# Kernel optimization log

Measured on AMD Instinct MI355X. Metric: run time of the kernel, lower is better.

Reference implementation:

```python
import jax, jax.numpy as jnp
import numpy as np
from jax.ops import segment_sum, segment_max

N = 20000   # nodes
E = 320000  # edges (no self loops; conv adds them)
G = 64      # graphs in batch
D = 128     # embed dim
H = 64      # GATConv out channels (heads=1)
L = 6       # number of conv/mlp blocks


def setup_inputs() -> dict:
    key = jax.random.key(0)
    ks = jax.random.split(key, 24)
    x_idx = jax.random.randint(ks[0], (N,), 0, 128)
    src = jax.random.randint(ks[1], (E,), 0, N)
    dst = jax.random.randint(ks[2], (E,), 0, N)
    dst = jnp.where(src == dst, (dst + 1) % N, dst)  # remove_self_loops semantics
    edge_index = jnp.stack([src, dst])
    edge_attr_idx = jax.random.randint(ks[3], (E,), 0, 128)
    batch = (jnp.arange(N) * G) // N  # sorted graph ids, ~312 nodes/graph
    s = 0.1
    r = lambda k, shp: jax.random.normal(k, shp, dtype=jnp.float32) * s
    return {
        'x_idx': x_idx, 'edge_index': edge_index, 'edge_attr_idx': edge_attr_idx, 'batch': batch,
        'emb': r(ks[4], (128, D)),
        'conv_W': r(ks[5], (L, D, H)), 'conv_We': r(ks[6], (L, D, H)),
        'conv_att_src': r(ks[7], (L, H)), 'conv_att_dst': r(ks[8], (L, H)),
        'conv_att_edge': r(ks[9], (L, H)), 'conv_b': jnp.zeros((L, H), jnp.float32),
        'mlp_W1': r(ks[10], (L, H, H)), 'mlp_b1': jnp.zeros((L, H), jnp.float32),
        'mlp_W2': r(ks[11], (L, H, H)), 'mlp_b2': jnp.zeros((L, H), jnp.float32),
        'mlp_W3': r(ks[12], (L, H, D)), 'mlp_b3': jnp.zeros((L, D), jnp.float32),
        'g1_W1': r(ks[13], (D, H)), 'g1_b1': jnp.zeros((H,), jnp.float32),
        'g1_W2': r(ks[14], (H, 1)), 'g1_b2': jnp.zeros((1,), jnp.float32),
        'g2_W1': r(ks[15], (D, H)), 'g2_b1': jnp.zeros((H,), jnp.float32),
        'g2_W2': r(ks[16], (H, D)), 'g2_b2': jnp.zeros((D,), jnp.float32),
        'p_W1': r(ks[17], (D, H)), 'p_b1': jnp.zeros((H,), jnp.float32),
        'p_W2': r(ks[18], (H, H)), 'p_b2': jnp.zeros((H,), jnp.float32),
        'p_W3': r(ks[19], (H, 1)), 'p_b3': jnp.zeros((1,), jnp.float32),
    }


def _mlp3(x, W1, b1, W2, b2, W3, b3):
    h = jax.nn.relu(x @ W1 + b1)
    h = jax.nn.relu(h @ W2 + b2)
    return h @ W3 + b3


def reference(x_idx, edge_index, edge_attr_idx, batch, emb, conv_W, conv_We,
              conv_att_src, conv_att_dst, conv_att_edge, conv_b,
              mlp_W1, mlp_b1, mlp_W2, mlp_b2, mlp_W3, mlp_b3,
              g1_W1, g1_b1, g1_W2, g1_b2, g2_W1, g2_b1, g2_W2, g2_b2,
              p_W1, p_b1, p_W2, p_b2, p_W3, p_b3):
    n = x_idx.shape[0]
    x = emb[x_idx]                 # [N,128]
    e = emb[edge_attr_idx]         # [E,128]
    src, dst = edge_index[0], edge_index[1]
    # add_self_loops with fill_value='mean': loop attr = mean of incoming edge attrs
    deg = segment_sum(jnp.ones((e.shape[0],), x.dtype), dst, num_segments=n)
    loop_attr = segment_sum(e, dst, num_segments=n) / jnp.maximum(deg, 1.0)[:, None]
    e_full = jnp.concatenate([e, loop_attr], axis=0)             # [E+N,128]
    ar = jnp.arange(n)
    src_f = jnp.concatenate([src, ar])
    dst_f = jnp.concatenate([dst, ar])

    def gat_conv(x, i):
        h = x @ conv_W[i]                       # [N,64]
        ep = e_full @ conv_We[i]                # [E+N,64]
        a_s = h @ conv_att_src[i]               # [N]
        a_d = h @ conv_att_dst[i]               # [N]
        a_e = ep @ conv_att_edge[i]             # [E+N]
        logit = jax.nn.leaky_relu(a_s[src_f] + a_d[dst_f] + a_e, 0.2)
        m = segment_max(logit, dst_f, num_segments=n)
        w = jnp.exp(logit - m[dst_f])
        denom = segment_sum(w, dst_f, num_segments=n)
        alpha = w / denom[dst_f]
        out = segment_sum(h[src_f] * alpha[:, None], dst_f, num_segments=n)
        return out + conv_b[i]

    jkn = []
    for i in range(L):  # dropout is identity at inference
        x = gat_conv(x, i)
        x = _mlp3(x, mlp_W1[i], mlp_b1[i], mlp_W2[i], mlp_b2[i], mlp_W3[i], mlp_b3[i])
        jkn.append(x)
    jkn = jnp.stack(jkn)                                  # [6,N,128]
    ms = jnp.sqrt(jnp.sum(jnp.square(jkn), axis=2))       # [6,N]
    ni = jnp.argmax(ms, axis=0)                           # [N]
    feature = jnp.take_along_axis(jkn, ni[None, :, None], axis=0)[0]  # [N,128]

    # per-graph attention pooling (vectorized over the per-graph loop)
    h1 = (jax.nn.relu(feature @ g1_W1 + g1_b1) @ g1_W2 + g1_b2)[:, 0]  # [N]
    m = segment_max(h1, batch, num_segments=G)
    w = jnp.exp(h1 - m[batch])
    attn = w / segment_sum(w, batch, num_segments=G)[batch]            # softmax per graph
    h2 = jax.nn.relu(feature @ g2_W1 + g2_b1) @ g2_W2 + g2_b2          # [N,128]
    counts = segment_sum(jnp.ones((n,), feature.dtype), batch, num_segments=G)
    hg = segment_sum(attn[:, None] * h2, batch, num_segments=G) / counts[:, None]  # [G,128]

    out = _mlp3(hg, p_W1, p_b1, p_W2, p_b2, p_W3, p_b3)   # [G,1]
    return out[:, 0]
```

## Files before the change

### kernel.cpp

```cpp
#include <hip/hip_runtime.h>
#include <math.h>

__device__ __forceinline__ float lrelu(float x){ return x > 0.0f ? x : 0.2f*x; }
__device__ __forceinline__ float bcastf(float v, int l){
    return __int_as_float(__builtin_amdgcn_readlane(__float_as_int(v), l));
}


__global__ void k_count(const int* __restrict__ dst, int* __restrict__ cnt, int E){
    int e = blockIdx.x*256 + threadIdx.x;
    if(e < E) atomicAdd(&cnt[dst[e]], 1);
}

__global__ __launch_bounds__(1024) void k_scan(const int* __restrict__ cnt, int* __restrict__ rowptr, int n){
    __shared__ int ws[16];
    __shared__ int carrysh;
    int t = threadIdx.x, lane = t & 63, wv = t >> 6;
    if(t==0){ carrysh = 0; rowptr[0] = 0; }
    __syncthreads();
    for(int base=0; base<n; base+=1024){
        int i = base + t;
        int v = (i<n) ? cnt[i] : 0;
        int s = v;
        #pragma unroll
        for(int off=1; off<64; off<<=1){ int u = __shfl_up(s, off, 64); if(lane>=off) s += u; }
        if(lane==63) ws[wv] = s;
        __syncthreads();
        if(t < 16){
            int u = ws[t];
            #pragma unroll
            for(int off=1; off<16; off<<=1){ int u2 = __shfl_up(u, off, 16); if(t>=off) u += u2; }
            ws[t] = u;
        }
        __syncthreads();
        int carry = carrysh;
        int wbase = wv ? ws[wv-1] : 0;
        if(i<n) rowptr[i+1] = carry + wbase + s;
        int total = ws[15];
        __syncthreads();
        if(t==0) carrysh = carry + total;
        __syncthreads();
    }
}

__global__ void k_scatter(const int* __restrict__ dst, const int* __restrict__ rowptr,
                          int* __restrict__ cnt2, int* __restrict__ eid, int E){
    int e = blockIdx.x*256 + threadIdx.x;
    if(e >= E) return;
    int d = dst[e];
    int p = rowptr[d] + atomicAdd(&cnt2[d], 1);
    eid[p] = e;
}

__global__ __launch_bounds__(256) void k_sortb(const int* __restrict__ rowptr, int* __restrict__ eid, int n){
    int node = blockIdx.x*4 + (threadIdx.x>>6);
    if(node >= n) return;
    int lane = threadIdx.x & 63;
    int b = rowptr[node], e = rowptr[node+1];
    int nj = e - b;
    if(nj <= 1) return;
    if(nj <= 64){
        int v = (lane < nj) ? eid[b+lane] : 0x7fffffff;
        for(int k=2; k<=64; k<<=1){
            for(int j=k>>1; j>0; j>>=1){
                int vv = __shfl_xor(v, j, 64);
                bool up = ((lane & k) == 0);
                bool lower = ((lane & j) == 0);
                int mn = min(v,vv), mx = max(v,vv);
                v = (lower == up) ? mn : mx;
            }
        }
        if(lane < nj) eid[b+lane] = v;
    } else if(lane == 0){
        for(int i=b+1; i<e; i++){
            int key = eid[i]; int j = i-1;
            while(j>=b && eid[j] > key){ eid[j+1] = eid[j]; j--; }
            eid[j+1] = key;
        }
    }
}

__global__ __launch_bounds__(256) void k_ae(const int* __restrict__ eid, const int* __restrict__ src,
                     const int* __restrict__ eattr, const float* __restrict__ emb,
                     const float* __restrict__ We, const float* __restrict__ atte,
                     int* __restrict__ csrsrc, float* __restrict__ ae, int E){
    __shared__ float wv[6*128];
    for(int i=threadIdx.x; i<768; i+=256){
        int l = i>>7, k = i&127;
        const float* w = We + ((size_t)l*128 + k)*64;
        const float* a = atte + l*64;
        float s = 0.f;
        #pragma unroll 8
        for(int c=0;c<64;c++) s += w[c]*a[c];
        wv[i] = s;
    }
    __syncthreads();
    int p = blockIdx.x*256 + threadIdx.x;
    if(p >= E) return;
    int e = eid[p];
    csrsrc[p] = src[e];
    const float4* er = (const float4*)(emb + (size_t)eattr[e]*128);
    float acc[6] = {0,0,0,0,0,0};
    for(int k=0;k<32;k++){
        float4 v = er[k];
        #pragma unroll
        for(int l=0;l<6;l++){
            const float* w = wv + l*128 + k*4;
            acc[l] += v.x*w[0] + v.y*w[1] + v.z*w[2] + v.w*w[3];
        }
    }
    #pragma unroll
    for(int l=0;l<6;l++) ae[(size_t)l*E + p] = acc[l];
}


__global__ __launch_bounds__(512) void k_hx(const int* __restrict__ xidx, const float* __restrict__ emb,
        const float* __restrict__ W, const float* __restrict__ atts, const float* __restrict__ attd,
        float* __restrict__ h, float* __restrict__ as_, float* __restrict__ ad_, int n){
    __shared__ float xs[64][129];
    __shared__ float hs[64][65];
    __shared__ float redA[8][64], redB[8][64];
    int base = blockIdx.x*64;
    int t = threadIdx.x;
    {
        int r = t>>3, c0 = (t&7)*16;
        if(base + r < n){
            const float4* srcp = (const float4*)(emb + (size_t)xidx[base+r]*128 + c0);
            #pragma unroll
            for(int q=0;q<4;q++){
                float4 v = srcp[q];
                xs[r][c0+q*4+0]=v.x; xs[r][c0+q*4+1]=v.y; xs[r][c0+q*4+2]=v.z; xs[r][c0+q*4+3]=v.w;
            }
        } else {
            #pragma unroll
            for(int q=0;q<16;q++) xs[r][c0+q] = 0.f;
        }
    }
    __syncthreads();
    int lane = t & 63;
    int wid = __builtin_amdgcn_readfirstlane(t >> 6);
    int cb = wid*8;
    float acc[8] = {0,0,0,0,0,0,0,0};
    for(int k=0;k<128;k++){
        float xv = xs[lane][k];
        #pragma unroll
        for(int cc=0;cc<8;cc++) acc[cc] = fmaf(xv, W[k*64 + cb + cc], acc[cc]);
    }
    float pa=0.f, pd=0.f;
    #pragma unroll
    for(int cc=0;cc<8;cc++){
        hs[lane][cb+cc] = acc[cc];
        pa += acc[cc]*atts[cb+cc];
        pd += acc[cc]*attd[cb+cc];
    }
    redA[wid][lane]=pa; redB[wid][lane]=pd;
    __syncthreads();
    {
        int r = t>>3, c0 = (t&7)*8;
        if(base + r < n){
            float* dst = h + (size_t)(base+r)*64 + c0;
            #pragma unroll
            for(int q=0;q<8;q++) dst[q] = hs[r][c0+q];
        }
    }
    if(t < 64 && base + t < n){
        float sa=0.f, sd=0.f;
        #pragma unroll
        for(int w=0;w<8;w++){ sa += redA[w][t]; sd += redB[w][t]; }
        as_[base+t] = sa; ad_[base+t] = sd;
    }
}


__global__ __launch_bounds__(256) void k_gat(const float* __restrict__ h,
        const float* __restrict__ as_, const float* __restrict__ ad_,
        const float* __restrict__ ae, const int* __restrict__ rowptr,
        const int* __restrict__ csrsrc, const float* __restrict__ bias,
        float* __restrict__ o, int n){
    int node = blockIdx.x*4 + (threadIdx.x>>6);
    if(node >= n) return;
    int lane = threadIdx.x & 63;
    int b = rowptr[node], e = rowptr[node+1];
    float adv = ad_[node];
    float m = -1e30f, d = 0.f, sumae = 0.f;
    float a0=0.f, a1=0.f, a2=0.f, a3=0.f;
    for(int j0=b; j0<e; j0+=64){
        int nj = min(64, e-j0);
        int sj = 0; float aev = 0.f, lg = -1e30f;
        if(lane < nj){
            sj  = csrsrc[j0+lane];
            aev = ae[j0+lane];
            lg  = lrelu(as_[sj] + adv + aev);
        }
        float cm = lg, sa = aev;
        #pragma unroll
        for(int off=32; off; off>>=1){ cm = fmaxf(cm, __shfl_xor(cm,off,64)); sa += __shfl_xor(sa,off,64); }
        sumae += sa;
        float nm = fmaxf(m, cm);
        float w = (lane<nj) ? expf(lg-nm) : 0.f;
        float ws = w;
        #pragma unroll
        for(int off=32; off; off>>=1) ws += __shfl_xor(ws,off,64);
        float scale = (m > -1e29f) ? expf(m-nm) : 0.f;
        d = d*scale + ws;
        a0*=scale; a1*=scale; a2*=scale; a3*=scale;
        int j = 0;
        for(; j+3<nj; j+=4){
            a0 = fmaf(bcastf(w,j+0), h[(size_t)__builtin_amdgcn_readlane(sj,j+0)*64 + lane], a0);
            a1 = fmaf(bcastf(w,j+1), h[(size_t)__builtin_amdgcn_readlane(sj,j+1)*64 + lane], a1);
            a2 = fmaf(bcastf(w,j+2), h[(size_t)__builtin_amdgcn_readlane(sj,j+2)*64 + lane], a2);
            a3 = fmaf(bcastf(w,j+3), h[(size_t)__builtin_amdgcn_readlane(sj,j+3)*64 + lane], a3);
        }
        for(; j<nj; j++)
            a0 = fmaf(bcastf(w,j), h[(size_t)__builtin_amdgcn_readlane(sj,j)*64 + lane], a0);
        m = nm;
    }
    int deg = e - b;
    float ael = sumae / fmaxf((float)deg, 1.f);
    float ls = lrelu(as_[node] + adv + ael);
    float nm = fmaxf(m, ls);
    float scale = (m > -1e29f) ? expf(m-nm) : 0.f;
    float wl = expf(ls-nm);
    d = d*scale + wl;
    float acc = (a0+a1)+(a2+a3);
    acc = acc*scale + wl*h[(size_t)node*64 + lane];
    o[(size_t)node*64 + lane] = acc/d + bias[lane];
}


__global__ __launch_bounds__(512) void k_dense(
    const float* __restrict__ o,
    const float* __restrict__ W1, const float* __restrict__ b1,
    const float* __restrict__ W2, const float* __restrict__ b2,
    const float* __restrict__ W3, const float* __restrict__ b3,
    float* __restrict__ bestF, float* __restrict__ bestMs, int layer,
    const float* __restrict__ Wn, const float* __restrict__ atts, const float* __restrict__ attd,
    float* __restrict__ hn, float* __restrict__ asn, float* __restrict__ adn_,
    const float* __restrict__ A, const float* __restrict__ g1b1,
    const float* __restrict__ w2, const float* __restrict__ g1b2,
    const float* __restrict__ B, const float* __restrict__ g2b1,
    const float* __restrict__ C, const float* __restrict__ g2b2,
    float* __restrict__ h1, float* __restrict__ h2,
    int n, int last)
{
    __shared__ float o_s[64][65];
    __shared__ float t1[64][65];
    __shared__ float xs[64][129];
    __shared__ float redA[8][64], redB[8][64];
    __shared__ unsigned char updf[64];
    int base = blockIdx.x*64;
    int t = threadIdx.x, lane = t & 63;
    int wid = __builtin_amdgcn_readfirstlane(t >> 6);

    {
        int r = t>>3, c0 = (t&7)*8;
        if(base + r < n){
            const float4* srcp = (const float4*)(o + (size_t)(base+r)*64 + c0);
            float4 v0 = srcp[0], v1 = srcp[1];
            o_s[r][c0+0]=v0.x; o_s[r][c0+1]=v0.y; o_s[r][c0+2]=v0.z; o_s[r][c0+3]=v0.w;
            o_s[r][c0+4]=v1.x; o_s[r][c0+5]=v1.y; o_s[r][c0+6]=v1.z; o_s[r][c0+7]=v1.w;
        } else {
            #pragma unroll
            for(int q=0;q<8;q++) o_s[r][c0+q] = 0.f;
        }
    }
    __syncthreads();

    {
        int cb = wid*8;
        float acc[8];
        #pragma unroll
        for(int cc=0;cc<8;cc++) acc[cc] = b1[cb+cc];
        for(int k=0;k<64;k++){
            float ov = o_s[lane][k];
            #pragma unroll
            for(int cc=0;cc<8;cc++) acc[cc] = fmaf(ov, W1[k*64 + cb + cc], acc[cc]);
        }
        #pragma unroll
        for(int cc=0;cc<8;cc++) t1[lane][cb+cc] = fmaxf(acc[cc], 0.f);
    }
    __syncthreads();

    {
        int cb = wid*8;
        float acc[8];
        #pragma unroll
        for(int cc=0;cc<8;cc++) acc[cc] = b2[cb+cc];
        for(int k=0;k<64;k++){
            float tv = t1[lane][k];
            #pragma unroll
            for(int cc=0;cc<8;cc++) acc[cc] = fmaf(tv, W2[k*64 + cb + cc], acc[cc]);
        }
        __syncthreads();
        #pragma unroll
        for(int cc=0;cc<8;cc++) o_s[lane][cb+cc] = fmaxf(acc[cc], 0.f);
    }
    __syncthreads();

    {
        int cb = wid*16;
        float acc[16];
        #pragma unroll
        for(int cc=0;cc<16;cc++) acc[cc] = b3[cb+cc];
        for(int k=0;k<64;k++){
            float tv = o_s[lane][k];
            #pragma unroll
            for(int cc=0;cc<16;cc++) acc[cc] = fmaf(tv, W3[k*128 + cb + cc], acc[cc]);
        }
        float ms = 0.f;
        #pragma unroll
        for(int cc=0;cc<16;cc++){ xs[lane][cb+cc] = acc[cc]; ms += acc[cc]*acc[cc]; }
        redA[wid][lane] = ms;
    }
    __syncthreads();

    if(t < 64){
        int node = base + t; bool u = false;
        if(node < n){
            float ms = 0.f;
            #pragma unroll
            for(int w=0;w<8;w++) ms += redA[w][t];
            u = (layer==0) || (ms > bestMs[node]);
            if(u) bestMs[node] = ms;
        }
        updf[t] = u ? 1 : 0;
    }
    __syncthreads();

    if(!last){
        {
            int r = t>>3, c0 = (t&7)*16;
            if(updf[r] && base + r < n){
                float* dst = bestF + (size_t)(base+r)*128 + c0;
                #pragma unroll
                for(int q=0;q<16;q++) dst[q] = xs[r][c0+q];
            }
        }
        {
            int cb = wid*8;
            float acc[8] = {0,0,0,0,0,0,0,0};
            for(int k=0;k<128;k++){
                float xv = xs[lane][k];
                #pragma unroll
                for(int cc=0;cc<8;cc++) acc[cc] = fmaf(xv, Wn[k*64 + cb + cc], acc[cc]);
            }
            float pa=0.f, pd=0.f;
            #pragma unroll
            for(int cc=0;cc<8;cc++){
                t1[lane][cb+cc] = acc[cc];
                pa += acc[cc]*atts[cb+cc];
                pd += acc[cc]*attd[cb+cc];
            }
            redA[wid][lane]=pa; redB[wid][lane]=pd;
        }
        __syncthreads();
        {
            int r = t>>3, c0 = (t&7)*8;
            if(base + r < n){
                float* dst = hn + (size_t)(base+r)*64 + c0;
                #pragma unroll
                for(int q=0;q<8;q++) dst[q] = t1[r][c0+q];
            }
        }
        if(t < 64 && base + t < n){
            float sa=0.f, sd=0.f;
            #pragma unroll
            for(int w=0;w<8;w++){ sa += redA[w][t]; sd += redB[w][t]; }
            asn[base+t] = sa; adn_[base+t] = sd;
        }
        return;
    }

    {
        int r = t>>3, c0 = (t&7)*16;
        if(!updf[r] && base + r < n){
            const float4* srcp = (const float4*)(bestF + (size_t)(base+r)*128 + c0);
            #pragma unroll
            for(int q=0;q<4;q++){
                float4 v = srcp[q];
                xs[r][c0+q*4+0]=v.x; xs[r][c0+q*4+1]=v.y; xs[r][c0+q*4+2]=v.z; xs[r][c0+q*4+3]=v.w;
            }
        }
    }
    __syncthreads();
    if(wid < 4){
        int cb = wid*16;
        float acc[16];
        #pragma unroll
        for(int cc=0;cc<16;cc++) acc[cc] = g1b1[cb+cc];
        for(int k=0;k<128;k++){
            float fv = xs[lane][k];
            #pragma unroll
            for(int cc=0;cc<16;cc++) acc[cc] = fmaf(fv, A[k*64 + cb + cc], acc[cc]);
        }
        float pp = 0.f;
        #pragma unroll
        for(int cc=0;cc<16;cc++) pp += fmaxf(acc[cc],0.f)*w2[cb+cc];
        redA[wid][lane] = pp;
    } else {
        int cb = (wid-4)*16;
        float acc[16];
        #pragma unroll
        for(int cc=0;cc<16;cc++) acc[cc] = g2b1[cb+cc];
        for(int k=0;k<128;k++){
            float fv = xs[lane][k];
            #pragma unroll
            for(int cc=0;cc<16;cc++) acc[cc] = fmaf(fv, B[k*64 + cb + cc], acc[cc]);
        }
        #pragma unroll
        for(int cc=0;cc<16;cc++) t1[lane][cb+cc] = fmaxf(acc[cc],0.f);
    }
    __syncthreads();
    if(t < 64 && base + t < n)
        h1[base+t] = redA[0][t]+redA[1][t]+redA[2][t]+redA[3][t] + g1b2[0];
    {
        int cb = wid*16;
        float acc[16];
        #pragma unroll
        for(int cc=0;cc<16;cc++) acc[cc] = g2b2[cb+cc];
        for(int k=0;k<64;k++){
            float tv = t1[lane][k];
            #pragma unroll
            for(int cc=0;cc<16;cc++) acc[cc] = fmaf(tv, C[k*128 + cb + cc], acc[cc]);
        }
        __syncthreads();
        #pragma unroll
        for(int cc=0;cc<16;cc++) xs[lane][cb+cc] = acc[cc];
    }
    __syncthreads();
    {
        int r = t>>3, c0 = (t&7)*16;
        if(base + r < n){
            float* dst = h2 + (size_t)(base+r)*128 + c0;
            #pragma unroll
            for(int q=0;q<16;q++) dst[q] = xs[r][c0+q];
        }
    }
}


__global__ __launch_bounds__(128) void k_pool2(const float* __restrict__ h1, const float* __restrict__ h2,
                      float* __restrict__ wbuf,
                      const float* __restrict__ pW1, const float* __restrict__ pb1,
                      const float* __restrict__ pW2, const float* __restrict__ pb2,
                      const float* __restrict__ pW3, const float* __restrict__ pb3,
                      float* __restrict__ out, int n, int G){
    __shared__ float sh[128];
    __shared__ float hgrow[128];
    int g = blockIdx.x, tid = threadIdx.x;
    int start = (g*n + G-1)/G, end = ((g+1)*n + G-1)/G;
    float lm = -1e30f;
    for(int i=start+tid; i<end; i+=128) lm = fmaxf(lm, h1[i]);
    sh[tid]=lm; __syncthreads();
    for(int off=64; off; off>>=1){ if(tid<off) sh[tid]=fmaxf(sh[tid],sh[tid+off]); __syncthreads(); }
    float m = sh[0]; __syncthreads();
    float lsum = 0.f;
    for(int i=start+tid; i<end; i+=128){ float w = expf(h1[i]-m); wbuf[i]=w; lsum+=w; }
    sh[tid]=lsum; __syncthreads();
    for(int off=64; off; off>>=1){ if(tid<off) sh[tid]+=sh[tid+off]; __syncthreads(); }
    float denom = sh[0];
    float a0=0.f,a1=0.f,a2=0.f,a3=0.f;
    int i = start;
    for(; i+3<end; i+=4){
        a0 = fmaf(wbuf[i+0], h2[(size_t)(i+0)*128 + tid], a0);
        a1 = fmaf(wbuf[i+1], h2[(size_t)(i+1)*128 + tid], a1);
        a2 = fmaf(wbuf[i+2], h2[(size_t)(i+2)*128 + tid], a2);
        a3 = fmaf(wbuf[i+3], h2[(size_t)(i+3)*128 + tid], a3);
    }
    for(; i<end; i++) a0 = fmaf(wbuf[i], h2[(size_t)i*128 + tid], a0);
    float acc = (a0+a1)+(a2+a3);
    hgrow[tid] = acc/denom/(float)(end-start);
    __syncthreads();
    if(tid < 64){
        float t1v = pb1[tid];
        for(int k=0;k<128;k++) t1v = fmaf(hgrow[k], pW1[k*64+tid], t1v);
        t1v = fmaxf(t1v, 0.f);
        float t2v = pb2[tid];
        for(int k=0;k<64;k++) t2v = fmaf(__shfl(t1v,k,64), pW2[k*64+tid], t2v);
        t2v = fmaxf(t2v, 0.f);
        float s = t2v * pW3[tid];
        #pragma unroll
        for(int off=32; off; off>>=1) s += __shfl_xor(s,off,64);
        if(tid==0) out[g] = s + pb3[0];
    }
}

extern "C" void kernel_launch(void* const* d_in, const int* in_sizes, int n_in,
                              void* d_out, int out_size, void* d_ws, size_t ws_size,
                              hipStream_t stream){
    const int*   x_idx   = (const int*)  d_in[0];
    const int*   eindex  = (const int*)  d_in[1];
    const int*   eattr   = (const int*)  d_in[2];
    const float* emb     = (const float*)d_in[4];
    const float* conv_W  = (const float*)d_in[5];
    const float* conv_We = (const float*)d_in[6];
    const float* att_src = (const float*)d_in[7];
    const float* att_dst = (const float*)d_in[8];
    const float* att_edg = (const float*)d_in[9];
    const float* conv_b  = (const float*)d_in[10];
    const float* mW1 = (const float*)d_in[11]; const float* mb1 = (const float*)d_in[12];
    const float* mW2 = (const float*)d_in[13]; const float* mb2 = (const float*)d_in[14];
    const float* mW3 = (const float*)d_in[15]; const float* mb3 = (const float*)d_in[16];
    const float* g1W1= (const float*)d_in[17]; const float* g1b1= (const float*)d_in[18];
    const float* g1W2= (const float*)d_in[19]; const float* g1b2= (const float*)d_in[20];
    const float* g2W1= (const float*)d_in[21]; const float* g2b1= (const float*)d_in[22];
    const float* g2W2= (const float*)d_in[23]; const float* g2b2= (const float*)d_in[24];
    const float* pW1 = (const float*)d_in[25]; const float* pb1 = (const float*)d_in[26];
    const float* pW2 = (const float*)d_in[27]; const float* pb2 = (const float*)d_in[28];
    const float* pW3 = (const float*)d_in[29]; const float* pb3 = (const float*)d_in[30];

    const int N = in_sizes[0];
    const int E = in_sizes[2];
    const int G = out_size;
    const int* src = eindex;
    const int* dst = eindex + E;
    const int NT = (N + 63) / 64;
    const int NW = (N + 3) / 4;

    char* p = (char*)d_ws;
    auto alloc = [&](size_t bytes)->void*{ void* r = (void*)p; p += (bytes + 255) & ~(size_t)255; return r; };
    float* h      = (float*)alloc((size_t)N*64*4);
    float* o      = (float*)alloc((size_t)N*64*4);
    float* bestF  = (float*)alloc((size_t)N*128*4);
    float* h2buf  = (float*)alloc((size_t)N*128*4);
    float* bestMs = (float*)alloc((size_t)N*4);
    float* as_    = (float*)alloc((size_t)N*4);
    float* ad_    = (float*)alloc((size_t)N*4);
    float* ae     = (float*)alloc((size_t)6*E*4);
    float* h1     = (float*)alloc((size_t)N*4);
    int*   cnt    = (int*)  alloc((size_t)N*4);
    int*   cnt2   = (int*)  alloc((size_t)N*4);
    int*   rowptr = (int*)  alloc((size_t)(N+1)*4);
    int*   eid    = (int*)  alloc((size_t)E*4);
    int*   csrsrc = (int*)  alloc((size_t)E*4);

    hipMemsetAsync(cnt,  0, (size_t)N*4, stream);
    hipMemsetAsync(cnt2, 0, (size_t)N*4, stream);

    k_count<<<(E+255)/256, 256, 0, stream>>>(dst, cnt, E);
    k_scan<<<1, 1024, 0, stream>>>(cnt, rowptr, N);
    k_scatter<<<(E+255)/256, 256, 0, stream>>>(dst, rowptr, cnt2, eid, E);
    k_sortb<<<NW, 256, 0, stream>>>(rowptr, eid, N);
    k_ae<<<(E+255)/256, 256, 0, stream>>>(eid, src, eattr, emb, conv_We, att_edg, csrsrc, ae, E);
    k_hx<<<NT, 512, 0, stream>>>(x_idx, emb, conv_W, att_src, att_dst, h, as_, ad_, N);

    for(int l=0; l<6; l++){
        int last = (l==5) ? 1 : 0;
        const float* Wn   = last ? conv_W  : conv_W  + (size_t)(l+1)*8192;
        const float* atsn = last ? att_src : att_src + (l+1)*64;
        const float* atdn = last ? att_dst : att_dst + (l+1)*64;
        k_gat<<<NW, 256, 0, stream>>>(h, as_, ad_, ae + (size_t)l*E, rowptr, csrsrc, conv_b + l*64, o, N);
        k_dense<<<NT, 512, 0, stream>>>(o,
            mW1 + (size_t)l*4096, mb1 + l*64, mW2 + (size_t)l*4096, mb2 + l*64,
            mW3 + (size_t)l*8192, mb3 + l*128,
            bestF, bestMs, l,
            Wn, atsn, atdn,
            h, as_, ad_,
            g1W1, g1b1, g1W2, g1b2, g2W1, g2b1, g2W2, g2b2,
            h1, h2buf,
            N, last);
    }

    k_pool2<<<G, 128, 0, stream>>>(h1, h2buf, bestMs,
            pW1, pb1, pW2, pb2, pW3, pb3, (float*)d_out, N, G);
}
```

Before: 480.9 us.

## Replace per-edge attention logits with table lookup and stage dense weights in LDS

Edge attention terms depend only on the edge attribute index, so a 6x128 lookup table replaces the per-edge 6xE array. k_gat reads a packed src|attr word per edge plus a shared-memory table entry, which removes the per-edge float stream. Separately, k_dense stages each weight matrix into shared memory in 4096-float chunks instead of reading weights from global memory in the inner loops, and the freed t1 buffer is replaced by register accumulators. The trade-off is more __syncthreads barriers and a 16 KB LDS staging buffer per block, and the packing assumes node ids fit in 17 bits.

```diff
diff --git a/kernel.cpp b/kernel.cpp
--- a/kernel.cpp
+++ b/kernel.cpp
@@ -80,37 +80,37 @@
     }
 }
 
-__global__ __launch_bounds__(256) void k_ae(const int* __restrict__ eid, const int* __restrict__ src,
-                     const int* __restrict__ eattr, const float* __restrict__ emb,
-                     const float* __restrict__ We, const float* __restrict__ atte,
-                     int* __restrict__ csrsrc, float* __restrict__ ae, int E){
-    __shared__ float wv[6*128];
-    for(int i=threadIdx.x; i<768; i+=256){
-        int l = i>>7, k = i&127;
+__global__ void k_pack(const int* __restrict__ eid, const int* __restrict__ src,
+                       const int* __restrict__ eattr, int* __restrict__ packed, int E){
+    int p = blockIdx.x*256 + threadIdx.x;
+    if(p >= E) return;
+    int e = eid[p];
+    packed[p] = src[e] | (eattr[e] << 17);
+}
+
+__global__ __launch_bounds__(768) void k_table(const float* __restrict__ We, const float* __restrict__ atte,
+                                               const float* __restrict__ emb, float* __restrict__ T){
+    __shared__ float wv[768];
+    int t = threadIdx.x;
+    {
+        int l = t>>7, k = t&127;
         const float* w = We + ((size_t)l*128 + k)*64;
         const float* a = atte + l*64;
         float s = 0.f;
         #pragma unroll 8
         for(int c=0;c<64;c++) s += w[c]*a[c];
-        wv[i] = s;
-    }
-    __syncthreads();
-    int p = blockIdx.x*256 + threadIdx.x;
-    if(p >= E) return;
-    int e = eid[p];
-    csrsrc[p] = src[e];
-    const float4* er = (const float4*)(emb + (size_t)eattr[e]*128);
-    float acc[6] = {0,0,0,0,0,0};
+        wv[t] = s;
+    }
+    __syncthreads();
+    int l = t>>7, a = t&127;
+    const float4* er = (const float4*)(emb + (size_t)a*128);
+    const float* w = wv + l*128;
+    float acc = 0.f;
     for(int k=0;k<32;k++){
         float4 v = er[k];
-        #pragma unroll
-        for(int l=0;l<6;l++){
-            const float* w = wv + l*128 + k*4;
-            acc[l] += v.x*w[0] + v.y*w[1] + v.z*w[2] + v.w*w[3];
-        }
-    }
-    #pragma unroll
-    for(int l=0;l<6;l++) ae[(size_t)l*E + p] = acc[l];
+        acc += v.x*w[k*4+0] + v.y*w[k*4+1] + v.z*w[k*4+2] + v.w*w[k*4+3];
+    }
+    T[l*128 + a] = acc;
 }
 
 
@@ -174,9 +174,12 @@
 
 __global__ __launch_bounds__(256) void k_gat(const float* __restrict__ h,
         const float* __restrict__ as_, const float* __restrict__ ad_,
-        const float* __restrict__ ae, const int* __restrict__ rowptr,
-        const int* __restrict__ csrsrc, const float* __restrict__ bias,
+        const float* __restrict__ T, const int* __restrict__ packed,
+        const int* __restrict__ rowptr, const float* __restrict__ bias,
         float* __restrict__ o, int n){
+    __shared__ float Tl[128];
+    if(threadIdx.x < 128) Tl[threadIdx.x] = T[threadIdx.x];
+    __syncthreads();
     int node = blockIdx.x*4 + (threadIdx.x>>6);
     if(node >= n) return;
     int lane = threadIdx.x & 63;
@@ -188,8 +191,9 @@
         int nj = min(64, e-j0);
         int sj = 0; float aev = 0.f, lg = -1e30f;
         if(lane < nj){
-            sj  = csrsrc[j0+lane];
-            aev = ae[j0+lane];
+            int pk = packed[j0+lane];
+            sj  = pk & 0x1FFFF;
+            aev = Tl[pk >> 17];
             lg  = lrelu(as_[sj] + adv + aev);
         }
         float cm = lg, sa = aev;
@@ -244,13 +248,24 @@
     int n, int last)
 {
     __shared__ float o_s[64][65];
-    __shared__ float t1[64][65];
     __shared__ float xs[64][129];
+    __shared__ float ws[4096];
     __shared__ float redA[8][64], redB[8][64];
     __shared__ unsigned char updf[64];
     int base = blockIdx.x*64;
     int t = threadIdx.x, lane = t & 63;
     int wid = __builtin_amdgcn_readfirstlane(t >> 6);
+
+    auto stage = [&](const float* __restrict__ src){
+        {
+            float4 v = *(const float4*)(src + t*4);
+            ws[t*4+0]=v.x; ws[t*4+1]=v.y; ws[t*4+2]=v.z; ws[t*4+3]=v.w;
+        }
+        {
+            float4 v = *(const float4*)(src + 2048 + t*4);
+            ws[2048+t*4+0]=v.x; ws[2048+t*4+1]=v.y; ws[2048+t*4+2]=v.z; ws[2048+t*4+3]=v.w;
+        }
+    };
 
     {
         int r = t>>3, c0 = (t&7)*8;
@@ -264,52 +279,74 @@
             for(int q=0;q<8;q++) o_s[r][c0+q] = 0.f;
         }
     }
-    __syncthreads();
-
+    stage(W1);
+    __syncthreads();
+
+    float accB[8];
     {
         int cb = wid*8;
-        float acc[8];
-        #pragma unroll
-        for(int cc=0;cc<8;cc++) acc[cc] = b1[cb+cc];
+        #pragma unroll
+        for(int cc=0;cc<8;cc++) accB[cc] = b1[cb+cc];
         for(int k=0;k<64;k++){
             float ov = o_s[lane][k];
             #pragma unroll
-            for(int cc=0;cc<8;cc++) acc[cc] = fmaf(ov, W1[k*64 + cb + cc], acc[cc]);
-        }
-        #pragma unroll
-        for(int cc=0;cc<8;cc++) t1[lane][cb+cc] = fmaxf(acc[cc], 0.f);
-    }
-    __syncthreads();
-
+            for(int cc=0;cc<8;cc++) accB[cc] = fmaf(ov, ws[k*64 + cb + cc], accB[cc]);
+        }
+    }
+    __syncthreads();
     {
         int cb = wid*8;
-        float acc[8];
-        #pragma unroll
-        for(int cc=0;cc<8;cc++) acc[cc] = b2[cb+cc];
-        for(int k=0;k<64;k++){
-            float tv = t1[lane][k];
-            #pragma unroll
-            for(int cc=0;cc<8;cc++) acc[cc] = fmaf(tv, W2[k*64 + cb + cc], acc[cc]);
-        }
-        __syncthreads();
-        #pragma unroll
-        for(int cc=0;cc<8;cc++) o_s[lane][cb+cc] = fmaxf(acc[cc], 0.f);
-    }
-    __syncthreads();
-
-    {
-        int cb = wid*16;
-        float acc[16];
-        #pragma unroll
-        for(int cc=0;cc<16;cc++) acc[cc] = b3[cb+cc];
+        #pragma unroll
+        for(int cc=0;cc<8;cc++) o_s[lane][cb+cc] = fmaxf(accB[cc], 0.f);
+    }
+    stage(W2);
+    __syncthreads();
+
+    float accC[8];
+    {
+        int cb = wid*8;
+        #pragma unroll
+        for(int cc=0;cc<8;cc++) accC[cc] = b2[cb+cc];
         for(int k=0;k<64;k++){
             float tv = o_s[lane][k];
             #pragma unroll
-            for(int cc=0;cc<16;cc++) acc[cc] = fmaf(tv, W3[k*128 + cb + cc], acc[cc]);
-        }
+            for(int cc=0;cc<8;cc++) accC[cc] = fmaf(tv, ws[k*64 + cb + cc], accC[cc]);
+        }
+    }
+    __syncthreads();
+    {
+        int cb = wid*8;
+        #pragma unroll
+        for(int cc=0;cc<8;cc++) o_s[lane][cb+cc] = fmaxf(accC[cc], 0.f);
+    }
+    stage(W3);
+    __syncthreads();
+
+    float accD[16];
+    int cb16 = wid*16;
+    {
+        #pragma unroll
+        for(int cc=0;cc<16;cc++) accD[cc] = b3[cb16+cc];
+        for(int k=0;k<32;k++){
+            float tv = o_s[lane][k];
+            #pragma unroll
+            for(int cc=0;cc<16;cc++) accD[cc] = fmaf(tv, ws[k*128 + cb16 + cc], accD[cc]);
+        }
+    }
+    __syncthreads();
+    stage(W3 + 4096);
+    __syncthreads();
+    {
+        for(int k=0;k<32;k++){
+            float tv = o_s[lane][k+32];
+            #pragma unroll
+            for(int cc=0;cc<16;cc++) accD[cc] = fmaf(tv, ws[k*128 + cb16 + cc], accD[cc]);
+        }
+    }
+    {
         float ms = 0.f;
         #pragma unroll
-        for(int cc=0;cc<16;cc++){ xs[lane][cb+cc] = acc[cc]; ms += acc[cc]*acc[cc]; }
+        for(int cc=0;cc<16;cc++) ms += accD[cc]*accD[cc];
         redA[wid][lane] = ms;
     }
     __syncthreads();
@@ -325,9 +362,14 @@
         }
         updf[t] = u ? 1 : 0;
     }
-    __syncthreads();
+    {
+        #pragma unroll
+        for(int cc=0;cc<16;cc++) xs[lane][cb16+cc] = accD[cc];
+    }
 
     if(!last){
+        stage(Wn);
+        __syncthreads();
         {
             int r = t>>3, c0 = (t&7)*16;
             if(updf[r] && base + r < n){
@@ -336,22 +378,38 @@
                 for(int q=0;q<16;q++) dst[q] = xs[r][c0+q];
             }
         }
+        float accF[8];
+        int cb = wid*8;
         {
-            int cb = wid*8;
-            float acc[8] = {0,0,0,0,0,0,0,0};
-            for(int k=0;k<128;k++){
+            #pragma unroll
+            for(int cc=0;cc<8;cc++) accF[cc] = 0.f;
+            for(int k=0;k<64;k++){
                 float xv = xs[lane][k];
                 #pragma unroll
-                for(int cc=0;cc<8;cc++) acc[cc] = fmaf(xv, Wn[k*64 + cb + cc], acc[cc]);
+                for(int cc=0;cc<8;cc++) accF[cc] = fmaf(xv, ws[k*64 + cb + cc], accF[cc]);
             }
-            float pa=0.f, pd=0.f;
-            #pragma unroll
-            for(int cc=0;cc<8;cc++){
-                t1[lane][cb+cc] = acc[cc];
-                pa += acc[cc]*atts[cb+cc];
-                pd += acc[cc]*attd[cb+cc];
+        }
+        __syncthreads();
+        stage(Wn + 4096);
+        __syncthreads();
+        {
+            for(int k=0;k<64;k++){
+                float xv = xs[lane][k+64];
+                #pragma unroll
+                for(int cc=0;cc<8;cc++) accF[cc] = fmaf(xv, ws[k*64 + cb + cc], accF[cc]);
             }
-            redA[wid][lane]=pa; redB[wid][lane]=pd;
+        }
+        float pa=0.f, pd=0.f;
+        #pragma unroll
+        for(int cc=0;cc<8;cc++){
+            pa += accF[cc]*atts[cb+cc];
+            pd += accF[cc]*attd[cb+cc];
+        }
+        redA[wid][lane]=pa; redB[wid][lane]=pd;
+        __syncthreads();
+        {
+            #pragma unroll
+            for(int cc=0;cc<8;cc++) o_s[lane][cb+cc] = accF[cc];
         }
         __syncthreads();
         {
@@ -359,7 +417,7 @@
             if(base + r < n){
                 float* dst = hn + (size_t)(base+r)*64 + c0;
                 #pragma unroll
-                for(int q=0;q<8;q++) dst[q] = t1[r][c0+q];
+                for(int q=0;q<8;q++) dst[q] = o_s[r][c0+q];
             }
         }
         if(t < 64 && base + t < n){
@@ -371,6 +429,8 @@
         return;
     }
 
+    stage(A);
+    __syncthreads();
     {
         int r = t>>3, c0 = (t&7)*16;
         if(!updf[r] && base + r < n){
@@ -383,49 +443,89 @@
         }
     }
     __syncthreads();
-    if(wid < 4){
-        int cb = wid*16;
-        float acc[16];
-        #pragma unroll
-        for(int cc=0;cc<16;cc++) acc[cc] = g1b1[cb+cc];
-        for(int k=0;k<128;k++){
+
+    int cb = wid*8;
+    float accP[8];
+    {
+        #pragma unroll
+        for(int cc=0;cc<8;cc++) accP[cc] = g1b1[cb+cc];
+        for(int k=0;k<64;k++){
             float fv = xs[lane][k];
             #pragma unroll
-            for(int cc=0;cc<16;cc++) acc[cc] = fmaf(fv, A[k*64 + cb + cc], acc[cc]);
+            for(int cc=0;cc<8;cc++) accP[cc] = fmaf(fv, ws[k*64 + cb + cc], accP[cc]);
+        }
+    }
+    __syncthreads();
+    stage(A + 4096);
+    __syncthreads();
+    {
+        for(int k=0;k<64;k++){
+            float fv = xs[lane][k+64];
+            #pragma unroll
+            for(int cc=0;cc<8;cc++) accP[cc] = fmaf(fv, ws[k*64 + cb + cc], accP[cc]);
         }
         float pp = 0.f;
         #pragma unroll
-        for(int cc=0;cc<16;cc++) pp += fmaxf(acc[cc],0.f)*w2[cb+cc];
+        for(int cc=0;cc<8;cc++) pp += fmaxf(accP[cc],0.f)*w2[cb+cc];
         redA[wid][lane] = pp;
-    } else {
-        int cb = (wid-4)*16;
-        float acc[16];
-        #pragma unroll
-        for(int cc=0;cc<16;cc++) acc[cc] = g2b1[cb+cc];
-        for(int k=0;k<128;k++){
+    }
+    __syncthreads();
+    if(t < 64 && base + t < n){
+        float s = 0.f;
+        #pragma unroll
+        for(int w=0;w<8;w++) s += redA[w][t];
+        h1[base+t] = s + g1b2[0];
+    }
+    stage(B);
+    __syncthreads();
+
+    float accQ[8];
+    {
+        #pragma unroll
+        for(int cc=0;cc<8;cc++) accQ[cc] = g2b1[cb+cc];
+        for(int k=0;k<64;k++){
             float fv = xs[lane][k];
             #pragma unroll
-            for(int cc=0;cc<16;cc++) acc[cc] = fmaf(fv, B[k*64 + cb + cc], acc[cc]);
-        }
-        #pragma unroll
-        for(int cc=0;cc<16;cc++) t1[lane][cb+cc] = fmaxf(acc[cc],0.f);
-    }
-    __syncthreads();
-    if(t < 64 && base + t < n)
-        h1[base+t] = redA[0][t]+redA[1][t]+redA[2][t]+redA[3][t] + g1b2[0];
-    {
-        int cb = wid*16;
-        float acc[16];
-        #pragma unroll
-        for(int cc=0;cc<16;cc++) acc[cc] = g2b2[cb+cc];
+            for(int cc=0;cc<8;cc++) accQ[cc] = fmaf(fv, ws[k*64 + cb + cc], accQ[cc]);
+        }
+    }
+    __syncthreads();
+    stage(B + 4096);
+    __syncthreads();
+    {
         for(int k=0;k<64;k++){
-            float tv = t1[lane][k];
-            #pragma unroll
-            for(int cc=0;cc<16;cc++) acc[cc] = fmaf(tv, C[k*128 + cb + cc], acc[cc]);
-        }
-        __syncthreads();
-        #pragma unroll
-        for(int cc=0;cc<16;cc++) xs[lane][cb+cc] = acc[cc];
+            float fv = xs[lane][k+64];
+            #pragma unroll
+            for(int cc=0;cc<8;cc++) accQ[cc] = fmaf(fv, ws[k*64 + cb + cc], accQ[cc]);
+        }
+        #pragma unroll
+        for(int cc=0;cc<8;cc++) o_s[lane][cb+cc] = fmaxf(accQ[cc], 0.f);
+    }
+    __syncthreads();
+    stage(C);
+    __syncthreads();
+
+    float accR[16];
+    {
+        #pragma unroll
+        for(int cc=0;cc<16;cc++) accR[cc] = g2b2[cb16+cc];
+        for(int k=0;k<32;k++){
+            float tv = o_s[lane][k];
+            #pragma unroll
+            for(int cc=0;cc<16;cc++) accR[cc] = fmaf(tv, ws[k*128 + cb16 + cc], accR[cc]);
+        }
+    }
+    __syncthreads();
+    stage(C + 4096);
+    __syncthreads();
+    {
+        for(int k=0;k<32;k++){
+            float tv = o_s[lane][k+32];
+            #pragma unroll
+            for(int cc=0;cc<16;cc++) accR[cc] = fmaf(tv, ws[k*128 + cb16 + cc], accR[cc]);
+        }
+        #pragma unroll
+        for(int cc=0;cc<16;cc++) xs[lane][cb16+cc] = accR[cc];
     }
     __syncthreads();
     {
@@ -526,13 +626,13 @@
     float* bestMs = (float*)alloc((size_t)N*4);
     float* as_    = (float*)alloc((size_t)N*4);
     float* ad_    = (float*)alloc((size_t)N*4);
-    float* ae     = (float*)alloc((size_t)6*E*4);
+    float* Tbuf   = (float*)alloc(6*128*4);
     float* h1     = (float*)alloc((size_t)N*4);
     int*   cnt    = (int*)  alloc((size_t)N*4);
     int*   cnt2   = (int*)  alloc((size_t)N*4);
     int*   rowptr = (int*)  alloc((size_t)(N+1)*4);
     int*   eid    = (int*)  alloc((size_t)E*4);
-    int*   csrsrc = (int*)  alloc((size_t)E*4);
+    int*   packed = (int*)  alloc((size_t)E*4);
 
     hipMemsetAsync(cnt,  0, (size_t)N*4, stream);
     hipMemsetAsync(cnt2, 0, (size_t)N*4, stream);
@@ -541,7 +641,8 @@
     k_scan<<<1, 1024, 0, stream>>>(cnt, rowptr, N);
     k_scatter<<<(E+255)/256, 256, 0, stream>>>(dst, rowptr, cnt2, eid, E);
     k_sortb<<<NW, 256, 0, stream>>>(rowptr, eid, N);
-    k_ae<<<(E+255)/256, 256, 0, stream>>>(eid, src, eattr, emb, conv_We, att_edg, csrsrc, ae, E);
+    k_pack<<<(E+255)/256, 256, 0, stream>>>(eid, src, eattr, packed, E);
+    k_table<<<1, 768, 0, stream>>>(conv_We, att_edg, emb, Tbuf);
     k_hx<<<NT, 512, 0, stream>>>(x_idx, emb, conv_W, att_src, att_dst, h, as_, ad_, N);
 
     for(int l=0; l<6; l++){
@@ -549,7 +650,7 @@
         const float* Wn   = last ? conv_W  : conv_W  + (size_t)(l+1)*8192;
         const float* atsn = last ? att_src : att_src + (l+1)*64;
         const float* atdn = last ? att_dst : att_dst + (l+1)*64;
-        k_gat<<<NW, 256, 0, stream>>>(h, as_, ad_, ae + (size_t)l*E, rowptr, csrsrc, conv_b + l*64, o, N);
+        k_gat<<<NW, 256, 0, stream>>>(h, as_, ad_, Tbuf + l*128, packed, rowptr, conv_b + l*64, o, N);
         k_dense<<<NT, 512, 0, stream>>>(o,
             mW1 + (size_t)l*4096, mb1 + l*64, mW2 + (size_t)l*4096, mb2 + l*64,
             mW3 + (size_t)l*8192, mb3 + l*128,
```

Result: slower. 540.8 us (+12.5%).

## Precompute per-attribute edge attention table and cut k_dense shared memory

Applied to the files above, without the earlier changes.

The edge attention logits depend only on the edge attribute index, so a single small kernel now builds a 6x128 table of emb·(We·att_edge) per layer and attribute. Per-edge work reduces to a table lookup, no longer a 128-wide dot product over the embedding row for each of the 320k edges. Separately, k_dense drops its t1 shared buffer and reuses o_s and xs as scratch, lowering LDS use to allow more resident blocks. This adds one tiny single-block kernel launch, and the buffer aliasing must respect the existing barriers.

```diff
diff --git a/kernel.cpp b/kernel.cpp
--- a/kernel.cpp
+++ b/kernel.cpp
@@ -80,37 +80,44 @@
     }
 }
 
-__global__ __launch_bounds__(256) void k_ae(const int* __restrict__ eid, const int* __restrict__ src,
-                     const int* __restrict__ eattr, const float* __restrict__ emb,
-                     const float* __restrict__ We, const float* __restrict__ atte,
-                     int* __restrict__ csrsrc, float* __restrict__ ae, int E){
-    __shared__ float wv[6*128];
-    for(int i=threadIdx.x; i<768; i+=256){
-        int l = i>>7, k = i&127;
+__global__ __launch_bounds__(768) void k_table(const float* __restrict__ We, const float* __restrict__ atte,
+                                               const float* __restrict__ emb, float* __restrict__ T){
+    __shared__ float wv[768];
+    int t = threadIdx.x;
+    {
+        int l = t>>7, k = t&127;
         const float* w = We + ((size_t)l*128 + k)*64;
         const float* a = atte + l*64;
         float s = 0.f;
         #pragma unroll 8
         for(int c=0;c<64;c++) s += w[c]*a[c];
-        wv[i] = s;
-    }
+        wv[t] = s;
+    }
+    __syncthreads();
+    int l = t>>7, a = t&127;
+    const float4* er = (const float4*)(emb + (size_t)a*128);
+    const float* w = wv + l*128;
+    float acc = 0.f;
+    for(int k=0;k<32;k++){
+        float4 v = er[k];
+        acc += v.x*w[k*4+0] + v.y*w[k*4+1] + v.z*w[k*4+2] + v.w*w[k*4+3];
+    }
+    T[l*128 + a] = acc;
+}
+
+__global__ __launch_bounds__(256) void k_ae2(const int* __restrict__ eid, const int* __restrict__ src,
+                     const int* __restrict__ eattr, const float* __restrict__ T,
+                     int* __restrict__ csrsrc, float* __restrict__ ae, int E){
+    __shared__ float Tl[768];
+    for(int i=threadIdx.x; i<768; i+=256) Tl[i] = T[i];
     __syncthreads();
     int p = blockIdx.x*256 + threadIdx.x;
     if(p >= E) return;
     int e = eid[p];
     csrsrc[p] = src[e];
-    const float4* er = (const float4*)(emb + (size_t)eattr[e]*128);
-    float acc[6] = {0,0,0,0,0,0};
-    for(int k=0;k<32;k++){
-        float4 v = er[k];
-        #pragma unroll
-        for(int l=0;l<6;l++){
-            const float* w = wv + l*128 + k*4;
-            acc[l] += v.x*w[0] + v.y*w[1] + v.z*w[2] + v.w*w[3];
-        }
-    }
+    int a = eattr[e];
     #pragma unroll
-    for(int l=0;l<6;l++) ae[(size_t)l*E + p] = acc[l];
+    for(int l=0;l<6;l++) ae[(size_t)l*E + p] = Tl[l*128 + a];
 }
 
 
@@ -244,7 +251,6 @@
     int n, int last)
 {
     __shared__ float o_s[64][65];
-    __shared__ float t1[64][65];
     __shared__ float xs[64][129];
     __shared__ float redA[8][64], redB[8][64];
     __shared__ unsigned char updf[64];
@@ -277,7 +283,7 @@
             for(int cc=0;cc<8;cc++) acc[cc] = fmaf(ov, W1[k*64 + cb + cc], acc[cc]);
         }
         #pragma unroll
-        for(int cc=0;cc<8;cc++) t1[lane][cb+cc] = fmaxf(acc[cc], 0.f);
+        for(int cc=0;cc<8;cc++) xs[lane][cb+cc] = fmaxf(acc[cc], 0.f);
     }
     __syncthreads();
 
@@ -287,7 +293,7 @@
         #pragma unroll
         for(int cc=0;cc<8;cc++) acc[cc] = b2[cb+cc];
         for(int k=0;k<64;k++){
-            float tv = t1[lane][k];
+            float tv = xs[lane][k];
             #pragma unroll
             for(int cc=0;cc<8;cc++) acc[cc] = fmaf(tv, W2[k*64 + cb + cc], acc[cc]);
         }
@@ -347,7 +353,7 @@
             float pa=0.f, pd=0.f;
             #pragma unroll
             for(int cc=0;cc<8;cc++){
-                t1[lane][cb+cc] = acc[cc];
+                o_s[lane][cb+cc] = acc[cc];
                 pa += acc[cc]*atts[cb+cc];
                 pd += acc[cc]*attd[cb+cc];
             }
@@ -359,7 +365,7 @@
             if(base + r < n){
                 float* dst = hn + (size_t)(base+r)*64 + c0;
                 #pragma unroll
-                for(int q=0;q<8;q++) dst[q] = t1[r][c0+q];
+                for(int q=0;q<8;q++) dst[q] = o_s[r][c0+q];
             }
         }
         if(t < 64 && base + t < n){
@@ -408,7 +414,7 @@
             for(int cc=0;cc<16;cc++) acc[cc] = fmaf(fv, B[k*64 + cb + cc], acc[cc]);
         }
         #pragma unroll
-        for(int cc=0;cc<16;cc++) t1[lane][cb+cc] = fmaxf(acc[cc],0.f);
+        for(int cc=0;cc<16;cc++) o_s[lane][cb+cc] = fmaxf(acc[cc],0.f);
     }
     __syncthreads();
     if(t < 64 && base + t < n)
@@ -419,7 +425,7 @@
         #pragma unroll
         for(int cc=0;cc<16;cc++) acc[cc] = g2b2[cb+cc];
         for(int k=0;k<64;k++){
-            float tv = t1[lane][k];
+            float tv = o_s[lane][k];
             #pragma unroll
             for(int cc=0;cc<16;cc++) acc[cc] = fmaf(tv, C[k*128 + cb + cc], acc[cc]);
         }
@@ -527,6 +533,7 @@
     float* as_    = (float*)alloc((size_t)N*4);
     float* ad_    = (float*)alloc((size_t)N*4);
     float* ae     = (float*)alloc((size_t)6*E*4);
+    float* Tbuf   = (float*)alloc(6*128*4);
     float* h1     = (float*)alloc((size_t)N*4);
     int*   cnt    = (int*)  alloc((size_t)N*4);
     int*   cnt2   = (int*)  alloc((size_t)N*4);
@@ -541,7 +548,8 @@
     k_scan<<<1, 1024, 0, stream>>>(cnt, rowptr, N);
     k_scatter<<<(E+255)/256, 256, 0, stream>>>(dst, rowptr, cnt2, eid, E);
     k_sortb<<<NW, 256, 0, stream>>>(rowptr, eid, N);
-    k_ae<<<(E+255)/256, 256, 0, stream>>>(eid, src, eattr, emb, conv_We, att_edg, csrsrc, ae, E);
+    k_table<<<1, 768, 0, stream>>>(conv_We, att_edg, emb, Tbuf);
+    k_ae2<<<(E+255)/256, 256, 0, stream>>>(eid, src, eattr, Tbuf, csrsrc, ae, E);
     k_hx<<<NT, 512, 0, stream>>>(x_idx, emb, conv_W, att_src, att_dst, h, as_, ad_, N);
 
     for(int l=0; l<6; l++){
```

After: 446.6 us. 1.08x faster.
